# Optimization experiments

Hardware: AMD Instinct MI355X
Metric: run time of the kernel (lower is better)

The kernel has to match this reference:

```python
import jax, jax.numpy as jnp
import numpy as np

B, DC, DB, DF = 16384, 2048, 768, 256
NF = DB  # num_features (isSwinT=True)
EPS = 1e-5


def setup_inputs() -> dict:
    key = jax.random.key(0)
    ks = jax.random.split(key, 20)
    s = 0.02
    return {
        'x_context': jax.random.normal(ks[0], (B, DC), jnp.float32),
        'x_body': jax.random.normal(ks[1], (B, DB), jnp.float32),
        'x_face': jax.random.normal(ks[2], (B, DF), jnp.float32),
        'Wc': jax.random.normal(ks[3], (NF, DC), jnp.float32) * s,
        'bc': jax.random.normal(ks[4], (NF,), jnp.float32) * s,
        'Wa1': jax.random.normal(ks[5], (128, NF), jnp.float32) * s,
        'ba1': jax.random.normal(ks[6], (128,), jnp.float32) * s,
        'ga': jnp.ones((128,), jnp.float32),
        'bba': jnp.zeros((128,), jnp.float32),
        'Wa2': jax.random.normal(ks[7], (1, 128), jnp.float32) * s,
        'ba2': jax.random.normal(ks[8], (1,), jnp.float32) * s,
        'W1': jax.random.normal(ks[9], (256, NF * 3), jnp.float32) * s,
        'b1': jax.random.normal(ks[10], (256,), jnp.float32) * s,
        'g1': jnp.ones((256,), jnp.float32),
        'be1': jnp.zeros((256,), jnp.float32),
        'Wcat': jax.random.normal(ks[11], (26, 256), jnp.float32) * s,
        'bcat': jax.random.normal(ks[12], (26,), jnp.float32) * s,
    }


def _bn(x, g, b):
    # BatchNorm1d, training mode (biased batch stats), deterministic
    m = jnp.mean(x, axis=0)
    v = jnp.mean((x - m) ** 2, axis=0)
    return (x - m) * jax.lax.rsqrt(v + EPS) * g + b


def reference(x_context, x_body, x_face, Wc, bc, Wa1, ba1, ga, bba, Wa2, ba2,
              W1, b1, g1, be1, Wcat, bcat):
    # face repeated elementwise to body width: [B,256,1]->repeat(3)->view[B,768]
    face = jnp.repeat(x_face, DB // DF, axis=1)              # [B, NF]
    ctx = x_context @ Wc.T + bc                              # [B, NF]
    body = x_body                                            # [B, NF]

    def cross_atten(a, u, v):
        # two 1x1 dot-products, softmax over size-2 dim, weighted sum
        d = jnp.stack([jnp.sum(a * u, axis=1), jnp.sum(a * v, axis=1)], axis=1)  # [B,2]
        att = jax.nn.softmax(d, axis=1)
        # sum over dim2 of a[:, :, None] @ att[:, None, :] == a * att.sum(1)
        return a * jnp.sum(att, axis=1, keepdims=True)

    cfeat = cross_atten(ctx, body, face)
    bfeat = cross_atten(body, ctx, face)
    ffeat = cross_atten(face, ctx, body)

    def fc_att(x):
        h = _bn(x @ Wa1.T + ba1, ga, bba)
        h = jax.nn.gelu(h, approximate=False)
        return h @ Wa2.T + ba2                               # [B, 1]

    score = jax.nn.softmax(
        jnp.concatenate([fc_att(cfeat), fc_att(bfeat), fc_att(ffeat)], axis=1), axis=1)  # [B,3]
    cfeat = cfeat * score[:, 0:1]
    bfeat = bfeat * score[:, 1:2]
    ffeat = ffeat * score[:, 2:3]

    fuse = jnp.concatenate([cfeat, bfeat, ffeat], axis=1) @ W1.T + b1  # [B,256]
    fuse = jax.nn.relu(_bn(fuse, g1, be1))  # dropout p=0.5 treated as identity (eval)
    return fuse @ Wcat.T + bcat             # [B,26]
```

## Files before the change

kernel.cpp:

```cpp
#include <hip/hip_runtime.h>
#include <hip/hip_bf16.h>
#include <stdint.h>

typedef float f32x4 __attribute__((ext_vector_type(4)));
typedef short bf16x8 __attribute__((ext_vector_type(8)));
typedef unsigned short u16;

static constexpr int kB  = 16384;
static constexpr int kDC = 2048;
static constexpr int kNF = 768;
static constexpr float kEps = 1e-5f;

static constexpr size_t OFF_FEATS  = 0;
static constexpr size_t OFF_X      = 75497472;
static constexpr size_t OFF_WCBF   = OFF_X + 67108864;
static constexpr size_t OFF_WA1BF  = OFF_WCBF + 3145728;
static constexpr size_t OFF_W1BF   = OFF_WA1BF + 196608;
static constexpr size_t OFF_FUSE   = OFF_W1BF + 1179648;
static constexpr size_t OFF_SCORES = OFF_FUSE + 16777216;
static constexpr size_t OFF_STATS  = OFF_SCORES + 196608;

static __device__ __forceinline__ u16 f2bf(float x) {
  union { float f; unsigned u; } c; c.f = x;
  unsigned r = c.u + 0x7fffu + ((c.u >> 16) & 1u);
  return (u16)(r >> 16);
}

static __device__ __forceinline__ unsigned pk2(float lo, float hi) {
  union { __hip_bfloat162 h; unsigned u; } c;
  c.h = __float22bfloat162_rn(make_float2(lo, hi));
  return c.u;
}

static __device__ __forceinline__ void cvtw(const float* __restrict__ in,
                                            u16* __restrict__ out, long u0) {
  float4 a[4], b[4];
#pragma unroll
  for (int i = 0; i < 4; ++i) {
    const long u = u0 + i * 256;
    a[i] = ((const float4*)in)[2 * u];
    b[i] = ((const float4*)in)[2 * u + 1];
  }
  __builtin_amdgcn_sched_barrier(0);
#pragma unroll
  for (int i = 0; i < 4; ++i) {
    const long u = u0 + i * 256;
    uint4 w;
    w.x = pk2(a[i].x, a[i].y); w.y = pk2(a[i].z, a[i].w);
    w.z = pk2(b[i].x, b[i].y); w.w = pk2(b[i].z, b[i].w);
    ((uint4*)out)[u] = w;
  }
}

__global__ __launch_bounds__(256) void prep_kernel(
    const float* __restrict__ xc, const float* __restrict__ Wc,
    const float* __restrict__ Wa1, const float* __restrict__ W1,
    u16* __restrict__ axbf, u16* __restrict__ wcbf,
    u16* __restrict__ wa1bf, u16* __restrict__ w1bf,
    float* __restrict__ stats)
{
  const int b = blockIdx.x, t = threadIdx.x;
  if (b == 4372) {
#pragma unroll
    for (int i = 0; i < 5; ++i) stats[t + i * 256] = 0.f;
    return;
  }
  const float* in; u16* out; long base;
  if (b < 4096)      { in = xc;  out = axbf;  base = (long)b * 1024 + t; }
  else if (b < 4288) { in = Wc;  out = wcbf;  base = (long)(b - 4096) * 1024 + t; }
  else if (b < 4300) { in = Wa1; out = wa1bf; base = (long)(b - 4288) * 1024 + t; }
  else               { in = W1;  out = w1bf;  base = (long)(b - 4300) * 1024 + t; }
  cvtw(in, out, base);
}

static __device__ __forceinline__ void gload16(const void* g, void* l) {
  __builtin_amdgcn_global_load_lds(
      (const __attribute__((address_space(1))) void*)g,
      (__attribute__((address_space(3))) void*)l, 16, 0, 0);
}

__global__ __launch_bounds__(256) void gemm_ctx_conv(
    const u16* __restrict__ A, const u16* __restrict__ B,
    const float* __restrict__ bias, u16* __restrict__ C,
    const float* __restrict__ xb, const float* __restrict__ xf,
    u16* __restrict__ feats)
{
  __shared__ __align__(16) u16 As[128 * 32];
  __shared__ __align__(16) u16 Bs[128 * 32];
  const int id = blockIdx.x, t = threadIdx.x;

  if (id >= 768) {
    const int c = id - 768;
    if (c < 1536) {
      cvtw(xb, feats + (size_t)kB * kNF, (long)c * 1024 + t);
    } else {
      const long base = (long)(c - 1536) * 1024 + t;
      float4 a[4], bb4[4];
#pragma unroll
      for (int i = 0; i < 4; ++i) {
        const long u = base + i * 256;
        a[i]   = ((const float4*)xf)[2 * u];
        bb4[i] = ((const float4*)xf)[2 * u + 1];
      }
      __builtin_amdgcn_sched_barrier(0);
#pragma unroll
      for (int i = 0; i < 4; ++i) {
        const long u = base + i * 256;
        const size_t row = (size_t)(u >> 5);
        const int col = (int)(u & 31) * 8;
        const float ax = a[i].x, ay = a[i].y, az = a[i].z, aw = a[i].w;
        const float bx = bb4[i].x, by = bb4[i].y, bz = bb4[i].z, bw = bb4[i].w;
        uint4* o = (uint4*)(feats + (size_t)2 * kB * kNF + row * kNF + (size_t)col * 3);
        uint4 w0, w1, w2;
        w0.x = pk2(ax, ax); w0.y = pk2(ax, ay); w0.z = pk2(ay, ay); w0.w = pk2(az, az);
        w1.x = pk2(az, aw); w1.y = pk2(aw, aw); w1.z = pk2(bx, bx); w1.w = pk2(bx, by);
        w2.x = pk2(by, by); w2.y = pk2(bz, bz); w2.z = pk2(bz, bw); w2.w = pk2(bw, bw);
        o[0] = w0; o[1] = w1; o[2] = w2;
      }
    }
    return;
  }

  const int bx = id & 127, by = id >> 7;
  const size_t m0 = (size_t)bx * 128;
  const int n0 = by * 128;
  const int lane = t & 63, wave = t >> 6;
  const int wm = (wave >> 1) * 64, wn = (wave & 1) * 64;
  const int fr = lane & 15, fq = lane >> 4;

  const int srow = t >> 2, scol = (t & 3) * 8;
  const u16* ga0 = A + (m0 + srow) * (size_t)kDC + scol;
  const u16* ga1 = A + (m0 + 64 + srow) * (size_t)kDC + scol;
  const u16* gb0 = B + (size_t)(n0 + srow) * kDC + scol;
  const u16* gb1 = B + (size_t)(n0 + 64 + srow) * kDC + scol;
  u16* la = As + t * 8;
  u16* lb = Bs + t * 8;
  const u16* fa = As + (wm + fr) * 32 + fq * 8;
  const u16* fb = Bs + (wn + fr) * 32 + fq * 8;

  f32x4 acc[4][4] = {};

  for (int k = 0; k < 64; ++k) {
    __syncthreads();
    gload16(ga0, la);
    gload16(ga1, la + 2048);
    gload16(gb0, lb);
    gload16(gb1, lb + 2048);
    ga0 += 32; ga1 += 32; gb0 += 32; gb1 += 32;
    __syncthreads();
    bf16x8 av[4], bv[4];
#pragma unroll
    for (int mf = 0; mf < 4; ++mf) av[mf] = *(const bf16x8*)(fa + mf * 512);
#pragma unroll
    for (int nf = 0; nf < 4; ++nf) bv[nf] = *(const bf16x8*)(fb + nf * 512);
#pragma unroll
    for (int mf = 0; mf < 4; ++mf)
#pragma unroll
      for (int nf = 0; nf < 4; ++nf)
        acc[mf][nf] = __builtin_amdgcn_mfma_f32_16x16x32_bf16(av[mf], bv[nf], acc[mf][nf], 0, 0, 0);
  }

#pragma unroll
  for (int mf = 0; mf < 4; ++mf) {
    const size_t rb = m0 + wm + mf * 16 + fq * 4;
#pragma unroll
    for (int nf = 0; nf < 4; ++nf) {
      const int gn = n0 + wn + nf * 16 + fr;
      const float bb = bias[gn];
#pragma unroll
      for (int rr = 0; rr < 4; ++rr)
        C[(rb + rr) * (size_t)kNF + gn] = f2bf(acc[mf][nf][rr] + bb);
    }
  }
}

template <int STATS>
__global__ __launch_bounds__(256) void gemm_bt64(
    const u16* __restrict__ A, int lda, const u16* __restrict__ B, int ldb,
    const float* __restrict__ bias, float* __restrict__ C, int ldc, int K,
    float* __restrict__ stats)
{
  __shared__ __align__(16) u16 As[2 * 64 * 32];
  __shared__ __align__(16) u16 Bs[2 * 128 * 32];
  const int bx = blockIdx.x, by = blockIdx.y;
  const size_t m0 = (size_t)bx * 64;
  const int n0 = by * 128;
  const int t = threadIdx.x;
  const int lane = t & 63, wave = t >> 6;
  const int wn = wave * 32;
  const int fr = lane & 15, fq = lane >> 4;

  const int srow = t >> 2, scol = (t & 3) * 8;
  const u16* ga0 = A + (m0 + srow) * (size_t)lda + scol;
  const u16* gb0 = B + (size_t)(n0 + srow) * ldb + scol;
  const u16* gb1 = B + (size_t)(n0 + 64 + srow) * ldb + scol;

  f32x4 acc[4][2] = {};

  gload16(ga0, As + t * 8);
  gload16(gb0, Bs + t * 8);
  gload16(gb1, Bs + t * 8 + 2048);
  ga0 += 32; gb0 += 32; gb1 += 32;
  __syncthreads();

  const int kt = K >> 5;
  for (int k = 0; k < kt; ++k) {
    const int cur = k & 1;
    if (k + 1 < kt) {
      u16* an = As + (cur ^ 1) * 2048;
      u16* bn = Bs + (cur ^ 1) * 4096;
      gload16(ga0, an + t * 8);
      gload16(gb0, bn + t * 8);
      gload16(gb1, bn + t * 8 + 2048);
      ga0 += 32; gb0 += 32; gb1 += 32;
    }
    const u16* fa = As + cur * 2048 + fr * 32 + fq * 8;
    const u16* fb = Bs + cur * 4096 + (wn + fr) * 32 + fq * 8;
    bf16x8 av[4], bv[2];
#pragma unroll
    for (int mf = 0; mf < 4; ++mf) av[mf] = *(const bf16x8*)(fa + mf * 512);
#pragma unroll
    for (int nf = 0; nf < 2; ++nf) bv[nf] = *(const bf16x8*)(fb + nf * 512);
#pragma unroll
    for (int mf = 0; mf < 4; ++mf)
#pragma unroll
      for (int nf = 0; nf < 2; ++nf)
        acc[mf][nf] = __builtin_amdgcn_mfma_f32_16x16x32_bf16(av[mf], bv[nf], acc[mf][nf], 0, 0, 0);
    __syncthreads();
  }

  float cs[2] = {}, cs2[2] = {};
#pragma unroll
  for (int mf = 0; mf < 4; ++mf) {
    const size_t rb = m0 + mf * 16 + fq * 4;
#pragma unroll
    for (int nf = 0; nf < 2; ++nf) {
      const int gn = n0 + wn + nf * 16 + fr;
      const float bb = bias[gn];
#pragma unroll
      for (int rr = 0; rr < 4; ++rr) {
        const float vv = acc[mf][nf][rr] + bb;
        C[(rb + rr) * (size_t)ldc + gn] = vv;
        if (STATS) { cs[nf] += vv; cs2[nf] += vv * vv; }
      }
    }
  }
  if (STATS) {
    const int f = (int)(m0 >> 14);
#pragma unroll
    for (int nf = 0; nf < 2; ++nf) {
      float s = cs[nf], s2 = cs2[nf];
      s += __shfl_down(s, 32); s2 += __shfl_down(s2, 32);
      s += __shfl_down(s, 16); s2 += __shfl_down(s2, 16);
      if (fq == 0) {
        const int gn = n0 + wn + nf * 16 + fr;
        atomicAdd(&stats[(f * 128 + gn) * 2 + 0], s);
        atomicAdd(&stats[(f * 128 + gn) * 2 + 1], s2);
      }
    }
  }
}

__global__ __launch_bounds__(256) void gemm_fuse64(
    const u16* __restrict__ feats, const u16* __restrict__ w1,
    const float* __restrict__ scores, const float* __restrict__ b1,
    float* __restrict__ fuse, float* __restrict__ fstats)
{
  __shared__ __align__(16) u16 As[2 * 64 * 32];
  __shared__ __align__(16) u16 Bs[2 * 128 * 32];
  const int bx = blockIdx.x, by = blockIdx.y;
  const size_t m0 = (size_t)bx * 64;
  const int n0 = by * 128;
  const int t = threadIdx.x;
  const int lane = t & 63, wave = t >> 6;
  const int wn = wave * 32;
  const int fr = lane & 15, fq = lane >> 4;
  const int srow = t >> 2, scol = (t & 3) * 8;

  const u16* ga0; const u16* gb0; const u16* gb1;
  auto setf = [&](int f) {
    ga0 = feats + (size_t)f * kB * kNF + (m0 + srow) * (size_t)kNF + scol;
    gb0 = w1 + f * kNF + (size_t)(n0 + srow) * 2304 + scol;
    gb1 = gb0 + (size_t)64 * 2304;
  };

  const f32x4 vzero = {};
  f32x4 acc[4][2] = {}, tot[4][2] = {};

  setf(0);
  gload16(ga0, As + t * 8);
  gload16(gb0, Bs + t * 8);
  gload16(gb1, Bs + t * 8 + 2048);
  ga0 += 32; gb0 += 32; gb1 += 32;
  int pf = 0, pk = 1;
  int ck = 0, cf = 0;
  __syncthreads();

  for (int s = 0; s < 72; ++s) {
    const int cur = s & 1;
    if (s < 71) {
      u16* an = As + (cur ^ 1) * 2048;
      u16* bn = Bs + (cur ^ 1) * 4096;
      gload16(ga0, an + t * 8);
      gload16(gb0, bn + t * 8);
      gload16(gb1, bn + t * 8 + 2048);
      if (++pk == 24) { pk = 0; ++pf; if (pf < 3) setf(pf); }
      else { ga0 += 32; gb0 += 32; gb1 += 32; }
    }
    const u16* fa = As + cur * 2048 + fr * 32 + fq * 8;
    const u16* fb = Bs + cur * 4096 + (wn + fr) * 32 + fq * 8;
    bf16x8 av[4], bv[2];
#pragma unroll
    for (int mf = 0; mf < 4; ++mf) av[mf] = *(const bf16x8*)(fa + mf * 512);
#pragma unroll
    for (int nf = 0; nf < 2; ++nf) bv[nf] = *(const bf16x8*)(fb + nf * 512);
#pragma unroll
    for (int mf = 0; mf < 4; ++mf)
#pragma unroll
      for (int nf = 0; nf < 2; ++nf)
        acc[mf][nf] = __builtin_amdgcn_mfma_f32_16x16x32_bf16(av[mf], bv[nf], acc[mf][nf], 0, 0, 0);
    if (++ck == 24) {
      ck = 0;
#pragma unroll
      for (int mf = 0; mf < 4; ++mf) {
        const size_t rb = m0 + mf * 16 + fq * 4;
#pragma unroll
        for (int rr = 0; rr < 4; ++rr) {
          const float sv = scores[(rb + rr) * 3 + cf];
#pragma unroll
          for (int nf = 0; nf < 2; ++nf) tot[mf][nf][rr] += sv * acc[mf][nf][rr];
        }
      }
#pragma unroll
      for (int mf = 0; mf < 4; ++mf)
#pragma unroll
        for (int nf = 0; nf < 2; ++nf) acc[mf][nf] = vzero;
      ++cf;
    }
    __syncthreads();
  }

  float cs[2] = {}, cs2[2] = {};
#pragma unroll
  for (int mf = 0; mf < 4; ++mf) {
    const size_t rb = m0 + mf * 16 + fq * 4;
#pragma unroll
    for (int nf = 0; nf < 2; ++nf) {
      const int gn = n0 + wn + nf * 16 + fr;
      const float bb = b1[gn];
#pragma unroll
      for (int rr = 0; rr < 4; ++rr) {
        const float vv = tot[mf][nf][rr] + bb;
        fuse[(rb + rr) * 256 + gn] = vv;
        cs[nf] += vv; cs2[nf] += vv * vv;
      }
    }
  }
#pragma unroll
  for (int nf = 0; nf < 2; ++nf) {
    float s = cs[nf], s2 = cs2[nf];
    s += __shfl_down(s, 32); s2 += __shfl_down(s2, 32);
    s += __shfl_down(s, 16); s2 += __shfl_down(s2, 16);
    if (fq == 0) {
      const int gn = n0 + wn + nf * 16 + fr;
      atomicAdd(&fstats[gn * 2 + 0], s);
      atomicAdd(&fstats[gn * 2 + 1], s2);
    }
  }
}

__global__ __launch_bounds__(64) void att_kernel(
    const float* __restrict__ H, const float* __restrict__ stats,
    const float* __restrict__ ga, const float* __restrict__ bba,
    const float* __restrict__ Wa2, const float* __restrict__ ba2,
    float* __restrict__ scores)
{
  const int i = blockIdx.x, l = threadIdx.x;
  float d[3];
#pragma unroll
  for (int f = 0; f < 3; ++f) {
    float part = 0.f;
#pragma unroll
    for (int h = 0; h < 2; ++h) {
      const int c = l + h * 64;
      const float sum = stats[(f * 128 + c) * 2 + 0];
      const float sq  = stats[(f * 128 + c) * 2 + 1];
      const float m = sum * (1.f / kB);
      const float var = sq * (1.f / kB) - m * m;
      const float rs = rsqrtf(var + kEps);
      const float x = H[((size_t)f * kB + i) * 128 + c];
      const float xn = (x - m) * rs * ga[c] + bba[c];
      const float ge = 0.5f * xn * (1.f + erff(xn * 0.70710678118f));
      part += ge * Wa2[c];
    }
#pragma unroll
    for (int off = 32; off > 0; off >>= 1) part += __shfl_down(part, off);
    d[f] = part;
  }
  if (l == 0) {
    const float b2 = ba2[0];
    float d0 = d[0] + b2, d1 = d[1] + b2, d2 = d[2] + b2;
    const float mx = fmaxf(d0, fmaxf(d1, d2));
    const float e0 = expf(d0 - mx), e1 = expf(d1 - mx), e2 = expf(d2 - mx);
    const float inv = 1.f / (e0 + e1 + e2);
    scores[i * 3 + 0] = e0 * inv;
    scores[i * 3 + 1] = e1 * inv;
    scores[i * 3 + 2] = e2 * inv;
  }
}

__global__ __launch_bounds__(64) void final_kernel(
    const float* __restrict__ fuse, const float* __restrict__ fstats,
    const float* __restrict__ g1, const float* __restrict__ be1,
    const float* __restrict__ Wcat, const float* __restrict__ bcat,
    float* __restrict__ out)
{
  const int i = blockIdx.x, l = threadIdx.x;
  __shared__ float row[256];
#pragma unroll
  for (int h = 0; h < 4; ++h) {
    const int c = l + h * 64;
    const float sum = fstats[c * 2 + 0], sq = fstats[c * 2 + 1];
    const float m = sum * (1.f / kB);
    const float var = sq * (1.f / kB) - m * m;
    const float rs = rsqrtf(var + kEps);
    const float v = (fuse[(size_t)i * 256 + c] - m) * rs * g1[c] + be1[c];
    row[c] = fmaxf(v, 0.f);
  }
  __syncthreads();
  if (l < 26) {
    float acc = bcat[l];
    const float* w = Wcat + l * 256;
    for (int k2 = 0; k2 < 256; ++k2) acc += row[k2] * w[k2];
    out[(size_t)i * 26 + l] = acc;
  }
}

extern "C" void kernel_launch(void* const* d_in, const int* in_sizes, int n_in,
                              void* d_out, int out_size, void* d_ws, size_t ws_size,
                              hipStream_t stream) {
  (void)in_sizes; (void)n_in; (void)out_size; (void)ws_size;
  const float* xc   = (const float*)d_in[0];
  const float* xb   = (const float*)d_in[1];
  const float* xf   = (const float*)d_in[2];
  const float* Wc   = (const float*)d_in[3];
  const float* bc   = (const float*)d_in[4];
  const float* Wa1  = (const float*)d_in[5];
  const float* ba1  = (const float*)d_in[6];
  const float* ga   = (const float*)d_in[7];
  const float* bba  = (const float*)d_in[8];
  const float* Wa2  = (const float*)d_in[9];
  const float* ba2  = (const float*)d_in[10];
  const float* W1   = (const float*)d_in[11];
  const float* b1   = (const float*)d_in[12];
  const float* g1   = (const float*)d_in[13];
  const float* be1  = (const float*)d_in[14];
  const float* Wcat = (const float*)d_in[15];
  const float* bcat = (const float*)d_in[16];
  float* out = (float*)d_out;

  char* ws = (char*)d_ws;
  u16* feats   = (u16*)(ws + OFF_FEATS);
  u16* axbf    = (u16*)(ws + OFF_X);
  float* H     = (float*)(ws + OFF_X);
  u16* wcbf    = (u16*)(ws + OFF_WCBF);
  u16* wa1bf   = (u16*)(ws + OFF_WA1BF);
  u16* w1bf    = (u16*)(ws + OFF_W1BF);
  float* fuse  = (float*)(ws + OFF_FUSE);
  float* scores= (float*)(ws + OFF_SCORES);
  float* hst   = (float*)(ws + OFF_STATS);
  float* fst   = (float*)(ws + OFF_STATS + 3072);

  prep_kernel<<<4373, 256, 0, stream>>>(xc, Wc, Wa1, W1, axbf, wcbf, wa1bf, w1bf, hst);
  gemm_ctx_conv<<<2816, 256, 0, stream>>>(axbf, wcbf, bc, feats, xb, xf, feats);
  gemm_bt64<1><<<dim3(768, 1), 256, 0, stream>>>(feats, kNF, wa1bf, kNF, ba1, H, 128, kNF, hst);
  att_kernel<<<kB, 64, 0, stream>>>(H, hst, ga, bba, Wa2, ba2, scores);
  gemm_fuse64<<<dim3(256, 2), 256, 0, stream>>>(feats, w1bf, scores, b1, fuse, fst);
  final_kernel<<<kB, 64, 0, stream>>>(fuse, fst, g1, be1, Wcat, bcat, out);
}
```

Baseline: 288.1 us.

## Fuse attention-score kernel into fuse GEMM prologue and move weight casts

Removes the separate att_kernel launch (16384 tiny blocks) by computing BN+GELU+Wa2 dot and 3-way softmax for each 64-row tile inside gemm_fuse64's prologue, keeping scores in shared memory. The Wa1/W1 bf16 conversions move from prep_kernel into the tail blocks of gemm_ctx_conv. This cuts one launch and the global scores round trip, at the cost of recomputing the score prologue in both column blocks (by=0,1), which doubles the erf work, and of adding a serial prologue before the GEMM main loop.

```diff
diff --git a/kernel.cpp b/kernel.cpp
--- a/kernel.cpp
+++ b/kernel.cpp
@@ -17,8 +17,7 @@
 static constexpr size_t OFF_WA1BF  = OFF_WCBF + 3145728;
 static constexpr size_t OFF_W1BF   = OFF_WA1BF + 196608;
 static constexpr size_t OFF_FUSE   = OFF_W1BF + 1179648;
-static constexpr size_t OFF_SCORES = OFF_FUSE + 16777216;
-static constexpr size_t OFF_STATS  = OFF_SCORES + 196608;
+static constexpr size_t OFF_STATS  = OFF_FUSE + 16777216;
 
 static __device__ __forceinline__ u16 f2bf(float x) {
   union { float f; unsigned u; } c; c.f = x;
@@ -54,23 +53,17 @@
 
 __global__ __launch_bounds__(256) void prep_kernel(
     const float* __restrict__ xc, const float* __restrict__ Wc,
-    const float* __restrict__ Wa1, const float* __restrict__ W1,
     u16* __restrict__ axbf, u16* __restrict__ wcbf,
-    u16* __restrict__ wa1bf, u16* __restrict__ w1bf,
     float* __restrict__ stats)
 {
   const int b = blockIdx.x, t = threadIdx.x;
-  if (b == 4372) {
+  if (b == 4288) {
 #pragma unroll
     for (int i = 0; i < 5; ++i) stats[t + i * 256] = 0.f;
     return;
   }
-  const float* in; u16* out; long base;
-  if (b < 4096)      { in = xc;  out = axbf;  base = (long)b * 1024 + t; }
-  else if (b < 4288) { in = Wc;  out = wcbf;  base = (long)(b - 4096) * 1024 + t; }
-  else if (b < 4300) { in = Wa1; out = wa1bf; base = (long)(b - 4288) * 1024 + t; }
-  else               { in = W1;  out = w1bf;  base = (long)(b - 4300) * 1024 + t; }
-  cvtw(in, out, base);
+  if (b < 4096) cvtw(xc, axbf, (long)b * 1024 + t);
+  else          cvtw(Wc, wcbf, (long)(b - 4096) * 1024 + t);
 }
 
 static __device__ __forceinline__ void gload16(const void* g, void* l) {
@@ -83,7 +76,8 @@
     const u16* __restrict__ A, const u16* __restrict__ B,
     const float* __restrict__ bias, u16* __restrict__ C,
     const float* __restrict__ xb, const float* __restrict__ xf,
-    u16* __restrict__ feats)
+    const float* __restrict__ Wa1, const float* __restrict__ W1,
+    u16* __restrict__ feats, u16* __restrict__ wa1bf, u16* __restrict__ w1bf)
 {
   __shared__ __align__(16) u16 As[128 * 32];
   __shared__ __align__(16) u16 Bs[128 * 32];
@@ -93,7 +87,7 @@
     const int c = id - 768;
     if (c < 1536) {
       cvtw(xb, feats + (size_t)kB * kNF, (long)c * 1024 + t);
-    } else {
+    } else if (c < 2048) {
       const long base = (long)(c - 1536) * 1024 + t;
       float4 a[4], bb4[4];
 #pragma unroll
@@ -117,6 +111,10 @@
         w2.x = pk2(by, by); w2.y = pk2(bz, bz); w2.z = pk2(bz, bw); w2.w = pk2(bw, bw);
         o[0] = w0; o[1] = w1; o[2] = w2;
       }
+    } else if (c < 2060) {
+      cvtw(Wa1, wa1bf, (long)(c - 2048) * 1024 + t);
+    } else {
+      cvtw(W1, w1bf, (long)(c - 2060) * 1024 + t);
     }
     return;
   }
@@ -263,11 +261,14 @@
 
 __global__ __launch_bounds__(256) void gemm_fuse64(
     const u16* __restrict__ feats, const u16* __restrict__ w1,
-    const float* __restrict__ scores, const float* __restrict__ b1,
-    float* __restrict__ fuse, float* __restrict__ fstats)
+    const float* __restrict__ H, const float* __restrict__ hst,
+    const float* __restrict__ ga, const float* __restrict__ bba,
+    const float* __restrict__ Wa2, const float* __restrict__ ba2,
+    const float* __restrict__ b1, float* __restrict__ fuse, float* __restrict__ fstats)
 {
   __shared__ __align__(16) u16 As[2 * 64 * 32];
   __shared__ __align__(16) u16 Bs[2 * 128 * 32];
+  __shared__ float gm[3][128], gb[3][128], wa2s[128], sc[64][4];
   const int bx = blockIdx.x, by = blockIdx.y;
   const size_t m0 = (size_t)bx * 64;
   const int n0 = by * 128;
@@ -276,6 +277,52 @@
   const int wn = wave * 32;
   const int fr = lane & 15, fq = lane >> 4;
   const int srow = t >> 2, scol = (t & 3) * 8;
+
+  if (t < 128) wa2s[t] = Wa2[t];
+  for (int e = t; e < 384; e += 256) {
+    const int f = e >> 7, c = e & 127;
+    const float m = hst[e * 2] * (1.f / kB);
+    const float var = hst[e * 2 + 1] * (1.f / kB) - m * m;
+    const float rs = rsqrtf(var + kEps) * ga[c];
+    gm[f][c] = rs;
+    gb[f][c] = bba[c] - m * rs;
+  }
+  __syncthreads();
+  {
+    const int pr = t >> 2, pq = t & 3;
+    const size_t prow = m0 + pr;
+    float d[3];
+#pragma unroll
+    for (int f = 0; f < 3; ++f) {
+      const float4* h4 = (const float4*)(H + ((size_t)f * kB + prow) * 128) + pq * 8;
+      float part = 0.f;
+#pragma unroll
+      for (int j = 0; j < 8; ++j) {
+        const float4 x = h4[j];
+        const int c = pq * 32 + j * 4;
+        const float xn0 = x.x * gm[f][c]     + gb[f][c];
+        const float xn1 = x.y * gm[f][c + 1] + gb[f][c + 1];
+        const float xn2 = x.z * gm[f][c + 2] + gb[f][c + 2];
+        const float xn3 = x.w * gm[f][c + 3] + gb[f][c + 3];
+        part += 0.5f * xn0 * (1.f + erff(xn0 * 0.70710678118f)) * wa2s[c];
+        part += 0.5f * xn1 * (1.f + erff(xn1 * 0.70710678118f)) * wa2s[c + 1];
+        part += 0.5f * xn2 * (1.f + erff(xn2 * 0.70710678118f)) * wa2s[c + 2];
+        part += 0.5f * xn3 * (1.f + erff(xn3 * 0.70710678118f)) * wa2s[c + 3];
+      }
+      part += __shfl_down(part, 2);
+      part += __shfl_down(part, 1);
+      d[f] = part;
+    }
+    if (pq == 0) {
+      const float b2 = ba2[0];
+      float d0 = d[0] + b2, d1 = d[1] + b2, d2 = d[2] + b2;
+      const float mx = fmaxf(d0, fmaxf(d1, d2));
+      const float e0 = expf(d0 - mx), e1 = expf(d1 - mx), e2 = expf(d2 - mx);
+      const float inv = 1.f / (e0 + e1 + e2);
+      sc[pr][0] = e0 * inv; sc[pr][1] = e1 * inv; sc[pr][2] = e2 * inv;
+    }
+  }
+  __syncthreads();
 
   const u16* ga0; const u16* gb0; const u16* gb1;
   auto setf = [&](int f) {
@@ -323,10 +370,10 @@
       ck = 0;
 #pragma unroll
       for (int mf = 0; mf < 4; ++mf) {
-        const size_t rb = m0 + mf * 16 + fq * 4;
+        const int rl = mf * 16 + fq * 4;
 #pragma unroll
         for (int rr = 0; rr < 4; ++rr) {
-          const float sv = scores[(rb + rr) * 3 + cf];
+          const float sv = sc[rl + rr][cf];
 #pragma unroll
           for (int nf = 0; nf < 2; ++nf) tot[mf][nf][rr] += sv * acc[mf][nf][rr];
         }
@@ -366,46 +413,6 @@
       atomicAdd(&fstats[gn * 2 + 0], s);
       atomicAdd(&fstats[gn * 2 + 1], s2);
     }
-  }
-}
-
-__global__ __launch_bounds__(64) void att_kernel(
-    const float* __restrict__ H, const float* __restrict__ stats,
-    const float* __restrict__ ga, const float* __restrict__ bba,
-    const float* __restrict__ Wa2, const float* __restrict__ ba2,
-    float* __restrict__ scores)
-{
-  const int i = blockIdx.x, l = threadIdx.x;
-  float d[3];
-#pragma unroll
-  for (int f = 0; f < 3; ++f) {
-    float part = 0.f;
-#pragma unroll
-    for (int h = 0; h < 2; ++h) {
-      const int c = l + h * 64;
-      const float sum = stats[(f * 128 + c) * 2 + 0];
-      const float sq  = stats[(f * 128 + c) * 2 + 1];
-      const float m = sum * (1.f / kB);
-      const float var = sq * (1.f / kB) - m * m;
-      const float rs = rsqrtf(var + kEps);
-      const float x = H[((size_t)f * kB + i) * 128 + c];
-      const float xn = (x - m) * rs * ga[c] + bba[c];
-      const float ge = 0.5f * xn * (1.f + erff(xn * 0.70710678118f));
-      part += ge * Wa2[c];
-    }
-#pragma unroll
-    for (int off = 32; off > 0; off >>= 1) part += __shfl_down(part, off);
-    d[f] = part;
-  }
-  if (l == 0) {
-    const float b2 = ba2[0];
-    float d0 = d[0] + b2, d1 = d[1] + b2, d2 = d[2] + b2;
-    const float mx = fmaxf(d0, fmaxf(d1, d2));
-    const float e0 = expf(d0 - mx), e1 = expf(d1 - mx), e2 = expf(d2 - mx);
-    const float inv = 1.f / (e0 + e1 + e2);
-    scores[i * 3 + 0] = e0 * inv;
-    scores[i * 3 + 1] = e1 * inv;
-    scores[i * 3 + 2] = e2 * inv;
   }
 }
 
@@ -467,14 +474,14 @@
   u16* wa1bf   = (u16*)(ws + OFF_WA1BF);
   u16* w1bf    = (u16*)(ws + OFF_W1BF);
   float* fuse  = (float*)(ws + OFF_FUSE);
-  float* scores= (float*)(ws + OFF_SCORES);
   float* hst   = (float*)(ws + OFF_STATS);
   float* fst   = (float*)(ws + OFF_STATS + 3072);
 
-  prep_kernel<<<4373, 256, 0, stream>>>(xc, Wc, Wa1, W1, axbf, wcbf, wa1bf, w1bf, hst);
-  gemm_ctx_conv<<<2816, 256, 0, stream>>>(axbf, wcbf, bc, feats, xb, xf, feats);
+  prep_kernel<<<4289, 256, 0, stream>>>(xc, Wc, axbf, wcbf, hst);
+  gemm_ctx_conv<<<2900, 256, 0, stream>>>(axbf, wcbf, bc, feats, xb, xf, Wa1, W1,
+                                          feats, wa1bf, w1bf);
   gemm_bt64<1><<<dim3(768, 1), 256, 0, stream>>>(feats, kNF, wa1bf, kNF, ba1, H, 128, kNF, hst);
-  att_kernel<<<kB, 64, 0, stream>>>(H, hst, ga, bba, Wa2, ba2, scores);
-  gemm_fuse64<<<dim3(256, 2), 256, 0, stream>>>(feats, w1bf, scores, b1, fuse, fst);
+  gemm_fuse64<<<dim3(256, 2), 256, 0, stream>>>(feats, w1bf, H, hst, ga, bba, Wa2, ba2,
+                                                b1, fuse, fst);
   final_kernel<<<kB, 64, 0, stream>>>(fuse, fst, g1, be1, Wcat, bcat, out);
 }
```

Result: no change. 289.5 us (+0.5%).
